# Kernel optimization log

Hardware: AMD Instinct MI355X
Metric: run time of the kernel (lower is better)

## Reference

```python
import jax, jax.numpy as jnp
import numpy as np

# Structure matrix S (n_hos*n_types=6, n_structures=8) and internal int_S (unused in forward)
S_MAT = np.array([[1,0,1,0,0,1,0,1],[0,1,0,1,1,0,0,0],[1,1,0,0,0,0,1,0],[0,0,1,1,0,1,0,0],[0,1,1,0,1,0,0,1],[1,0,0,0,1,0,1,0]], dtype=np.float32)
CONTROL_STRENGTH = 10.0  # self.control_strength
PDHG_ITERS = 150         # fixed-iteration batched primal-dual LP solver
BATCH = 32768
N_STRUCT = 8
N_COMBO = 6


def setup_inputs() -> dict:
    key = jax.random.key(0)
    ks = jax.random.split(key, 9)
    X = jax.random.uniform(ks[0], (BATCH, 2, 3), jnp.float32)  # nonnegative bids
    def lin(k, fan_in, fan_out):
        return jax.random.normal(k, (fan_in, fan_out), jnp.float32) * (1.0 / np.sqrt(fan_in))
    W1 = lin(ks[1], 6, 20);  b1 = jnp.zeros((20,), jnp.float32)
    W2 = lin(ks[2], 20, 20); b2 = jnp.zeros((20,), jnp.float32)
    W3 = lin(ks[3], 20, 20); b3 = jnp.zeros((20,), jnp.float32)
    W4 = lin(ks[4], 20, 8);  b4 = jnp.zeros((8,), jnp.float32)
    S = jnp.asarray(S_MAT)
    return {"X": X, "W1": W1, "b1": b1, "W2": W2, "b2": b2, "W3": W3, "b3": b3,
            "W4": W4, "b4": b4, "S": S, "batch_size": BATCH}


def _mlp(Z, W1, b1, W2, b2, W3, b3, W4, b4):
    h = jnp.tanh(Z @ W1 + b1)
    h = jnp.tanh(h @ W2 + b2)
    h = jnp.tanh(h @ W3 + b3)
    return h @ W4 + b4  # [B, 8]


def _batched_lp(S, z, bvec):
    """Solve, per batch row: max 1'x - c*||x - z||_2  s.t. x>=0, S x <= b.
    Equivalent polytope A x <= b' with A=[S; -I], b'=[b; 0]; solved with PDHG.
    z, bvec: [B, 8], [B, 6]."""
    B = z.shape[0]
    A = jnp.concatenate([S, -jnp.eye(N_STRUCT, dtype=S.dtype)], axis=0)  # [14, 8]
    bfull = jnp.concatenate([bvec, jnp.zeros((B, N_STRUCT), bvec.dtype)], axis=1)  # [B, 14]
    L = jnp.linalg.norm(A)  # Frobenius norm upper-bounds spectral norm
    tau = 1.0 / L
    sigma = 1.0 / L

    def prox_g(v):
        # prox of g(x) = -1'x + c||x - z||_2 (w = ones): shift by tau*w then shrink toward z
        u = v + tau
        d = u - z
        n = jnp.linalg.norm(d, axis=-1, keepdims=True)
        scale = jnp.maximum(0.0, 1.0 - tau * CONTROL_STRENGTH / jnp.maximum(n, 1e-12))
        return z + scale * d

    x0 = jnp.maximum(z, 0.0)
    y0 = jnp.zeros((B, N_COMBO + N_STRUCT), z.dtype)

    def step(carry, _):
        x, xbar, y = carry
        y = jnp.maximum(0.0, y + sigma * (xbar @ A.T - bfull))  # dual ascent + proj >= 0
        x_new = prox_g(x - tau * (y @ A))                        # primal prox step
        return (x_new, 2.0 * x_new - x, y), None

    (x, _, _), _ = jax.lax.scan(step, (x0, x0, y0), None, length=PDHG_ITERS)
    return x


def reference(X, W1, b1, W2, b2, W3, b3, W4, b4, S, batch_size):
    B = X.shape[0]
    Z = X.reshape(B, N_COMBO)              # view(-1, n_hos*n_types)
    z = _mlp(Z, W1, b1, W2, b2, W3, b3, W4, b4)  # neural_net_forward -> [B, 8]
    x1 = _batched_lp(S, z, Z)              # linear_program_forward (W = ones)
    return x1
```

## Files before the change

kernel.cpp:

```cpp
#include <hip/hip_runtime.h>
#include <math.h>


#define N_ITERS 150
typedef float f2 __attribute__((ext_vector_type(2)));
typedef float f4 __attribute__((ext_vector_type(4)));

__device__ __forceinline__ float fast_tanh(float a) {
    float e = __expf(2.0f * a);
    return 1.0f - 2.0f * __builtin_amdgcn_rcpf(e + 1.0f);
}

__device__ __forceinline__ float dpp_swap(float v) {
    union { float f; int i; } u;
    u.f = v;
    u.i = __builtin_amdgcn_update_dpp(0, u.i, 0xB1, 0xF, 0xF, true);
    return u.f;
}

__global__ void __launch_bounds__(64)
__attribute__((amdgpu_waves_per_eu(2)))
matchnet_kernel(
    const float* __restrict__ X,
    const float* __restrict__ W1, const float* __restrict__ b1,
    const float* __restrict__ W2, const float* __restrict__ b2,
    const float* __restrict__ W3, const float* __restrict__ b3,
    const float* __restrict__ W4, const float* __restrict__ b4,
    float* __restrict__ out, int B)
{
    __shared__ alignas(16) float tW1[160], tW2[400], tW3[400], tW4[160];
    __shared__ alignas(16) float sb1[20], sb2[20], sb3[20], sb4[8];
    {
        int tid = threadIdx.x;
        for (int idx = tid; idx < 120; idx += 64) { int i = idx / 20, j = idx % 20; tW1[j * 8 + i] = W1[idx]; }
        for (int idx = tid; idx < 400; idx += 64) { int i = idx / 20, j = idx % 20; tW2[j * 20 + i] = W2[idx]; }
        for (int idx = tid; idx < 400; idx += 64) { int i = idx / 20, j = idx % 20; tW3[j * 20 + i] = W3[idx]; }
        for (int idx = tid; idx < 160; idx += 64) { int i = idx / 8,  k = idx % 8;  tW4[k * 20 + i] = W4[idx]; }
        if (tid < 20) { sb1[tid] = b1[tid]; sb2[tid] = b2[tid]; sb3[tid] = b3[tid]; }
        if (tid < 8) sb4[tid] = b4[tid];
    }
    __syncthreads();

    int gidx = blockIdx.x * blockDim.x + threadIdx.x;
    int row  = gidx >> 2;
    if (row >= B) return;
    int sub = gidx & 3;
    const bool isOdd = (sub & 1) != 0;
    const bool isPairA = (sub < 2);
    const int jb = isOdd ? 10 : 0;
    const int kb = isOdd ? 4 : 0;

    float bb0 = X[row * 6 + 0], bb1 = X[row * 6 + 1], bb2 = X[row * 6 + 2];
    float bb3 = X[row * 6 + 3], bb4 = X[row * 6 + 4], bb5 = X[row * 6 + 5];

    float hA[10], hB[10];
    {
        float acc[10];
        const f2* bv = (const f2*)&sb1[jb];
        #pragma unroll
        for (int p = 0; p < 5; p++) { f2 b = bv[p]; acc[2 * p] = b.x; acc[2 * p + 1] = b.y; }
        #pragma unroll
        for (int n = 0; n < 10; n++) {
            int j = jb + n;
            f4 w0 = *(const f4*)&tW1[j * 8];
            f2 w1 = *(const f2*)&tW1[j * 8 + 4];
            float a = acc[n];
            a = fmaf(bb0, w0.x, a); a = fmaf(bb1, w0.y, a); a = fmaf(bb2, w0.z, a);
            a = fmaf(bb3, w0.w, a); a = fmaf(bb4, w1.x, a); a = fmaf(bb5, w1.y, a);
            acc[n] = fast_tanh(a);
        }
        #pragma unroll
        for (int n = 0; n < 10; n++) {
            float t = dpp_swap(acc[n]);
            hA[n] = isOdd ? t : acc[n];
            hB[n] = isOdd ? acc[n] : t;
        }
    }
    #pragma unroll
    for (int layer = 0; layer < 2; layer++) {
        const float* tw = layer ? tW3 : tW2;
        const float* sb = layer ? sb3 : sb2;
        float acc[10];
        const f2* bv = (const f2*)&sb[jb];
        #pragma unroll
        for (int p = 0; p < 5; p++) { f2 b = bv[p]; acc[2 * p] = b.x; acc[2 * p + 1] = b.y; }
        #pragma unroll
        for (int n = 0; n < 10; n++) {
            int j = jb + n;
            const f4* w = (const f4*)&tw[j * 20];
            f4 w0 = w[0], w1 = w[1], w2 = w[2], w3 = w[3], w4 = w[4];
            float a = acc[n];
            a = fmaf(hA[0], w0.x, a); a = fmaf(hA[1], w0.y, a);
            a = fmaf(hA[2], w0.z, a); a = fmaf(hA[3], w0.w, a);
            a = fmaf(hA[4], w1.x, a); a = fmaf(hA[5], w1.y, a);
            a = fmaf(hA[6], w1.z, a); a = fmaf(hA[7], w1.w, a);
            a = fmaf(hA[8], w2.x, a); a = fmaf(hA[9], w2.y, a);
            a = fmaf(hB[0], w2.z, a); a = fmaf(hB[1], w2.w, a);
            a = fmaf(hB[2], w3.x, a); a = fmaf(hB[3], w3.y, a);
            a = fmaf(hB[4], w3.z, a); a = fmaf(hB[5], w3.w, a);
            a = fmaf(hB[6], w4.x, a); a = fmaf(hB[7], w4.y, a);
            a = fmaf(hB[8], w4.z, a); a = fmaf(hB[9], w4.w, a);
            acc[n] = fast_tanh(a);
        }
        #pragma unroll
        for (int n = 0; n < 10; n++) {
            float t = dpp_swap(acc[n]);
            hA[n] = isOdd ? t : acc[n];
            hB[n] = isOdd ? acc[n] : t;
        }
    }
    float oz0, oz1, oz2, oz3;
    {
        f4 b = *(const f4*)&sb4[kb];
        float acc[4] = {b.x, b.y, b.z, b.w};
        #pragma unroll
        for (int n = 0; n < 4; n++) {
            int k = kb + n;
            const f4* w = (const f4*)&tW4[k * 20];
            f4 w0 = w[0], w1 = w[1], w2 = w[2], w3 = w[3], w4 = w[4];
            float a = acc[n];
            a = fmaf(hA[0], w0.x, a); a = fmaf(hA[1], w0.y, a);
            a = fmaf(hA[2], w0.z, a); a = fmaf(hA[3], w0.w, a);
            a = fmaf(hA[4], w1.x, a); a = fmaf(hA[5], w1.y, a);
            a = fmaf(hA[6], w1.z, a); a = fmaf(hA[7], w1.w, a);
            a = fmaf(hA[8], w2.x, a); a = fmaf(hA[9], w2.y, a);
            a = fmaf(hB[0], w2.z, a); a = fmaf(hB[1], w2.w, a);
            a = fmaf(hB[2], w3.x, a); a = fmaf(hB[3], w3.y, a);
            a = fmaf(hB[4], w3.z, a); a = fmaf(hB[5], w3.w, a);
            a = fmaf(hB[6], w4.x, a); a = fmaf(hB[7], w4.y, a);
            a = fmaf(hB[8], w4.z, a); a = fmaf(hB[9], w4.w, a);
            acc[n] = a;
        }
        oz0 = acc[0]; oz1 = acc[1]; oz2 = acc[2]; oz3 = acc[3];
    }

    const float tau  = 0.18898223650461363f;
    const float c    = 0.03571428571428571f;
    const float tauC = 1.8898223650461363f;

    float ot0 = tau - oz0, ot1 = tau - oz1, ot2 = tau - oz2, ot3 = tau - oz3;
    float oTI0 = ot0, oTI1 = ot1, oTI2 = ot2, oTI3 = ot3;

    float ox0 = fmaxf(oz0, 0.f), ox1 = fmaxf(oz1, 0.f);
    float ox2 = fmaxf(oz2, 0.f), ox3 = fmaxf(oz3, 0.f);
    float oxb0 = ox0, oxb1 = ox1, oxb2 = ox2, oxb3 = ox3;

    float cb0 = c * bb0, cb1 = c * bb1, cb2 = c * bb2;
    float cb3 = c * bb3, cb4 = c * bb4, cb5 = c * bb5;
    float cbq0 = isOdd ? cb4 : cb0;
    float cbq1 = isOdd ? cb3 : cb2;
    float cbq2 = isOdd ? cb5 : cb1;
    float Yq0 = 0.f, Yq1 = 0.f, Yq2 = 0.f;

    #pragma unroll 1
    for (int it = 0; it < N_ITERS; it++) {
        float rxb0 = dpp_swap(oxb0), rxb1 = dpp_swap(oxb1);
        float rxb2 = dpp_swap(oxb2), rxb3 = dpp_swap(oxb3);

        float op_a = oxb0 + rxb1;
        float op_b = oxb2 + rxb3;
        float op_c = oxb3 + rxb2;
        float op_d = isOdd ? op_c : op_b;
        float sq0  = op_a + op_d;
        float op_e = oxb1 + rxb2;
        float op_f = isOdd ? rxb3 : oxb0;
        float sq1  = op_e + op_f;
        float op_g = oxb1 + oxb3;
        float op_h = oxb0 + oxb2;
        float op_i = isOdd ? op_h : op_g;
        float sq2  = op_i + rxb0;

        Yq0 = fmaxf(0.f, fmaf(c, sq0, Yq0) - cbq0);
        Yq1 = fmaxf(0.f, fmaf(c, sq1, Yq1) - cbq1);
        Yq2 = fmaxf(0.f, fmaf(c, sq2, Yq2) - cbq2);

        float rY0 = dpp_swap(Yq0), rY1 = dpp_swap(Yq1), rY2 = dpp_swap(Yq2);

        float op_j = Yq0 + rY2;
        float op_k = isOdd ? Yq2 : Yq1;
        float colq0 = op_j + op_k;
        float op_l = Yq1 + rY0;
        float op_p = isOdd ? 0.f : Yq2;
        float colq1 = op_l + op_p;
        float op_m = Yq0 + rY0;
        float op_n = rY1 + Yq2;
        float op_o = op_m + rY1;
        float colq2 = isOdd ? op_n : op_o;
        float colq3 = isOdd ? op_m : op_n;

        oTI0 = fmaxf(ot0, fmaf(-c, oxb0, oTI0));
        oTI1 = fmaxf(ot1, fmaf(-c, oxb1, oTI1));
        oTI2 = fmaxf(ot2, fmaf(-c, oxb2, oTI2));
        oTI3 = fmaxf(ot3, fmaf(-c, oxb3, oTI3));

        float od0 = (ox0 + oTI0) - colq0;
        float od1 = (ox1 + oTI1) - colq1;
        float od2 = (ox2 + oTI2) - colq2;
        float od3 = (ox3 + oTI3) - colq3;

        float nl = od0 * od0;
        nl = fmaf(od1, od1, nl);
        nl = fmaf(od2, od2, nl);
        nl = fmaf(od3, od3, nl);
        float rn = dpp_swap(nl);
        float nsq = nl + rn;

        float rs = __builtin_amdgcn_rsqf(nsq);
        float scale = fmaxf(0.f, fmaf(-tauC, rs, 1.f));

        float xn0 = fmaf(scale, od0, oz0);
        float xn1 = fmaf(scale, od1, oz1);
        float xn2 = fmaf(scale, od2, oz2);
        float xn3 = fmaf(scale, od3, oz3);
        oxb0 = fmaf(2.f, xn0, -ox0); ox0 = xn0;
        oxb1 = fmaf(2.f, xn1, -ox1); ox1 = xn1;
        oxb2 = fmaf(2.f, xn2, -ox2); ox2 = xn2;
        oxb3 = fmaf(2.f, xn3, -ox3); ox3 = xn3;
    }

    if (isPairA) {
        float4* out4 = (float4*)out;
        out4[row * 2 + (isOdd ? 1 : 0)] = make_float4(ox0, ox1, ox2, ox3);
    }
}

extern "C" void kernel_launch(void* const* d_in, const int* in_sizes, int n_in,
                              void* d_out, int out_size, void* d_ws, size_t ws_size,
                              hipStream_t stream) {
    const float* X  = (const float*)d_in[0];
    const float* W1 = (const float*)d_in[1];
    const float* b1 = (const float*)d_in[2];
    const float* W2 = (const float*)d_in[3];
    const float* b2 = (const float*)d_in[4];
    const float* W3 = (const float*)d_in[5];
    const float* b3 = (const float*)d_in[6];
    const float* W4 = (const float*)d_in[7];
    const float* b4 = (const float*)d_in[8];
    float* out = (float*)d_out;

    int B = in_sizes[0] / 6;
    const int block = 64;
    long long threads = (long long)B * 4;
    int grid = (int)((threads + block - 1) / block);
    hipLaunchKernelGGL(matchnet_kernel, dim3(grid), dim3(block), 0, stream,
                       X, W1, b1, W2, b2, W3, b3, W4, b4, out, B);
}
```

Before: 118.6 us.

## Split PDHG iteration across four lanes per row with quad DPP permutes

Before, the four lanes of a row did redundant work in pairs: each pair held 4 primal components, and two lanes repeated the same computation. The PDHG loop now spreads each row's 8 primal and 6 dual variables across all four lanes, two primal and up to two dual per lane, using quad-permute DPP moves for the A and A^T products and for the norm reduction. This cuts per-lane ALU work in the serial 150-iteration loop. In exchange it adds more cross-lane permutes and per-lane selects, and the waves-per-EU hint now also sets a maximum of 2.

After: 111.9 us. -5.7%, faster.

```diff
diff --git a/kernel.cpp b/kernel.cpp
--- a/kernel.cpp
+++ b/kernel.cpp
@@ -11,15 +11,17 @@
     return 1.0f - 2.0f * __builtin_amdgcn_rcpf(e + 1.0f);
 }
 
-__device__ __forceinline__ float dpp_swap(float v) {
+template <int CTRL>
+__device__ __forceinline__ float qperm(float v) {
     union { float f; int i; } u;
     u.f = v;
-    u.i = __builtin_amdgcn_update_dpp(0, u.i, 0xB1, 0xF, 0xF, true);
+    u.i = __builtin_amdgcn_update_dpp(0, u.i, CTRL, 0xF, 0xF, true);
     return u.f;
 }
+#define QP(a,b,c,d) ((a) | ((b)<<2) | ((c)<<4) | ((d)<<6))
 
 __global__ void __launch_bounds__(64)
-__attribute__((amdgpu_waves_per_eu(2)))
+__attribute__((amdgpu_waves_per_eu(2, 2)))
 matchnet_kernel(
     const float* __restrict__ X,
     const float* __restrict__ W1, const float* __restrict__ b1,
@@ -44,11 +46,17 @@
     int gidx = blockIdx.x * blockDim.x + threadIdx.x;
     int row  = gidx >> 2;
     if (row >= B) return;
-    int sub = gidx & 3;
-    const bool isOdd = (sub & 1) != 0;
-    const bool isPairA = (sub < 2);
-    const int jb = isOdd ? 10 : 0;
-    const int kb = isOdd ? 4 : 0;
+    const int  sub     = gidx & 3;
+    const bool pairOdd = (sub & 1) != 0;
+    const bool isL1  = (sub == 1);
+    const bool isL2  = (sub == 2);
+    const bool isL3  = (sub == 3);
+    const bool isL12 = (sub == 1) || (sub == 2);
+    const bool isL23 = (sub >= 2);
+    const bool isL13 = isL1 || isL3;
+    const bool notL0 = (sub != 0);
+    const int jb = pairOdd ? 10 : 0;
+    const int kb = pairOdd ? 4 : 0;
 
     float bb0 = X[row * 6 + 0], bb1 = X[row * 6 + 1], bb2 = X[row * 6 + 2];
     float bb3 = X[row * 6 + 3], bb4 = X[row * 6 + 4], bb5 = X[row * 6 + 5];
@@ -71,9 +79,9 @@
         }
         #pragma unroll
         for (int n = 0; n < 10; n++) {
-            float t = dpp_swap(acc[n]);
-            hA[n] = isOdd ? t : acc[n];
-            hB[n] = isOdd ? acc[n] : t;
+            float t = qperm<QP(1,0,3,2)>(acc[n]);
+            hA[n] = pairOdd ? t : acc[n];
+            hB[n] = pairOdd ? acc[n] : t;
         }
     }
     #pragma unroll
@@ -104,9 +112,9 @@
         }
         #pragma unroll
         for (int n = 0; n < 10; n++) {
-            float t = dpp_swap(acc[n]);
-            hA[n] = isOdd ? t : acc[n];
-            hB[n] = isOdd ? acc[n] : t;
+            float t = qperm<QP(1,0,3,2)>(acc[n]);
+            hA[n] = pairOdd ? t : acc[n];
+            hB[n] = pairOdd ? acc[n] : t;
         }
     }
     float oz0, oz1, oz2, oz3;
@@ -134,94 +142,88 @@
         oz0 = acc[0]; oz1 = acc[1]; oz2 = acc[2]; oz3 = acc[3];
     }
 
+    float za, zb;
+    {
+        float dZ1 = qperm<QP(0,0,3,3)>(oz2);
+        float dZ2 = qperm<QP(3,3,3,3)>(oz0);
+        float t   = isL3 ? oz2 : oz0;
+        t  = isL1 ? dZ1 : t;
+        za = isL2 ? dZ2 : t;
+        float dZ3 = qperm<QP(0,0,0,0)>(oz3);
+        float dZ4 = qperm<QP(3,3,3,3)>(oz1);
+        float u   = isL3 ? oz3 : oz1;
+        u  = isL1 ? dZ3 : u;
+        zb = isL2 ? dZ4 : u;
+    }
+
     const float tau  = 0.18898223650461363f;
     const float c    = 0.03571428571428571f;
     const float tauC = 1.8898223650461363f;
 
-    float ot0 = tau - oz0, ot1 = tau - oz1, ot2 = tau - oz2, ot3 = tau - oz3;
-    float oTI0 = ot0, oTI1 = ot1, oTI2 = ot2, oTI3 = ot3;
-
-    float ox0 = fmaxf(oz0, 0.f), ox1 = fmaxf(oz1, 0.f);
-    float ox2 = fmaxf(oz2, 0.f), ox3 = fmaxf(oz3, 0.f);
-    float oxb0 = ox0, oxb1 = ox1, oxb2 = ox2, oxb3 = ox3;
-
     float cb0 = c * bb0, cb1 = c * bb1, cb2 = c * bb2;
     float cb3 = c * bb3, cb4 = c * bb4, cb5 = c * bb5;
-    float cbq0 = isOdd ? cb4 : cb0;
-    float cbq1 = isOdd ? cb3 : cb2;
-    float cbq2 = isOdd ? cb5 : cb1;
-    float Yq0 = 0.f, Yq1 = 0.f, Yq2 = 0.f;
+    float cb1q = isL1 ? cb1 : cb0;  cb1q = isL2 ? cb4 : cb1q;  cb1q = isL3 ? cb5 : cb1q;
+    float cb2q = isL1 ? cb3 : cb2;
+
+    float ta = tau - za, tb = tau - zb;
+    float TIa = ta, TIb = tb;
+    float xa = fmaxf(za, 0.f), xb_ = fmaxf(zb, 0.f);
+    float xba = xa, xbb = xb_;
+    float Y1 = 0.f, Y2 = 0.f;
 
     #pragma unroll 1
     for (int it = 0; it < N_ITERS; it++) {
-        float rxb0 = dpp_swap(oxb0), rxb1 = dpp_swap(oxb1);
-        float rxb2 = dpp_swap(oxb2), rxb3 = dpp_swap(oxb3);
-
-        float op_a = oxb0 + rxb1;
-        float op_b = oxb2 + rxb3;
-        float op_c = oxb3 + rxb2;
-        float op_d = isOdd ? op_c : op_b;
-        float sq0  = op_a + op_d;
-        float op_e = oxb1 + rxb2;
-        float op_f = isOdd ? rxb3 : oxb0;
-        float sq1  = op_e + op_f;
-        float op_g = oxb1 + oxb3;
-        float op_h = oxb0 + oxb2;
-        float op_i = isOdd ? op_h : op_g;
-        float sq2  = op_i + rxb0;
-
-        Yq0 = fmaxf(0.f, fmaf(c, sq0, Yq0) - cbq0);
-        Yq1 = fmaxf(0.f, fmaf(c, sq1, Yq1) - cbq1);
-        Yq2 = fmaxf(0.f, fmaf(c, sq2, Yq2) - cbq2);
-
-        float rY0 = dpp_swap(Yq0), rY1 = dpp_swap(Yq1), rY2 = dpp_swap(Yq2);
-
-        float op_j = Yq0 + rY2;
-        float op_k = isOdd ? Yq2 : Yq1;
-        float colq0 = op_j + op_k;
-        float op_l = Yq1 + rY0;
-        float op_p = isOdd ? 0.f : Yq2;
-        float colq1 = op_l + op_p;
-        float op_m = Yq0 + rY0;
-        float op_n = rY1 + Yq2;
-        float op_o = op_m + rY1;
-        float colq2 = isOdd ? op_n : op_o;
-        float colq3 = isOdd ? op_m : op_n;
-
-        oTI0 = fmaxf(ot0, fmaf(-c, oxb0, oTI0));
-        oTI1 = fmaxf(ot1, fmaf(-c, oxb1, oTI1));
-        oTI2 = fmaxf(ot2, fmaf(-c, oxb2, oTI2));
-        oTI3 = fmaxf(ot3, fmaf(-c, oxb3, oTI3));
-
-        float od0 = (ox0 + oTI0) - colq0;
-        float od1 = (ox1 + oTI1) - colq1;
-        float od2 = (ox2 + oTI2) - colq2;
-        float od3 = (ox3 + oTI3) - colq3;
-
-        float nl = od0 * od0;
-        nl = fmaf(od1, od1, nl);
-        nl = fmaf(od2, od2, nl);
-        nl = fmaf(od3, od3, nl);
-        float rn = dpp_swap(nl);
-        float nsq = nl + rn;
+        float dA1 = qperm<QP(1,2,1,0)>(xba);
+        float dA2 = qperm<QP(2,2,2,2)>(xba);
+        float dB1 = qperm<QP(2,0,0,0)>(xbb);
+        float dB2 = qperm<QP(3,3,3,3)>(xbb);
+        float P = isL1 ? xbb : xba;
+        float R = isL3 ? dA2 : dB1;
+        float T = isL13 ? 0.f : dB2;
+        float s1 = (P + dA1) + (R + T);
+        float dA3 = qperm<QP(3,3,3,3)>(xba);
+        float dB3 = qperm<QP(2,2,2,2)>(xbb);
+        float V = isL1 ? dB3 : dA3;
+        float s2 = (xba + xbb) + V;
+
+        Y1 = fmaxf(0.f, fmaf(c, s1, Y1) - cb1q);
+        Y2 = fmaxf(0.f, fmaf(c, s2, Y2) - cb2q);
+
+        float gYa = qperm<QP(3,0,1,0)>(Y1);
+        float gYb = qperm<QP(1,2,3,2)>(Y1);
+        float gYc = qperm<QP(2,2,0,0)>(Y1);
+        float gY2 = qperm<QP(1,0,1,0)>(Y2);
+        float T1 = isL12 ? gYa : Y1;  T1 = isL3 ? gY2 : T1;
+        float T2 = isL23 ? Y1  : Y2;
+        float T3 = isL12 ? gYb : gYa; T3 = isL3 ? 0.f : T3;
+        float colA = (T1 + T2) + T3;
+        float U1 = isL1 ? Y1  : gYb;  U1 = isL2 ? gYc : U1;  U1 = isL3 ? gYa : U1;
+        float U2 = isL2 ? gY2 : Y2;   U2 = isL3 ? gYb : U2;
+        float U3 = notL0 ? 0.f : gYc;
+        float colB = (U1 + U2) + U3;
+
+        TIa = fmaxf(ta, fmaf(-c, xba, TIa));
+        TIb = fmaxf(tb, fmaf(-c, xbb, TIb));
+
+        float da = (xa  + TIa) - colA;
+        float db = (xb_ + TIb) - colB;
+
+        float p  = fmaf(db, db, da * da);
+        float pp = p + qperm<QP(1,0,3,2)>(p);
+        float nsq = pp + qperm<QP(2,3,0,1)>(pp);
 
         float rs = __builtin_amdgcn_rsqf(nsq);
         float scale = fmaxf(0.f, fmaf(-tauC, rs, 1.f));
 
-        float xn0 = fmaf(scale, od0, oz0);
-        float xn1 = fmaf(scale, od1, oz1);
-        float xn2 = fmaf(scale, od2, oz2);
-        float xn3 = fmaf(scale, od3, oz3);
-        oxb0 = fmaf(2.f, xn0, -ox0); ox0 = xn0;
-        oxb1 = fmaf(2.f, xn1, -ox1); ox1 = xn1;
-        oxb2 = fmaf(2.f, xn2, -ox2); ox2 = xn2;
-        oxb3 = fmaf(2.f, xn3, -ox3); ox3 = xn3;
-    }
-
-    if (isPairA) {
-        float4* out4 = (float4*)out;
-        out4[row * 2 + (isOdd ? 1 : 0)] = make_float4(ox0, ox1, ox2, ox3);
-    }
+        float xna = fmaf(scale, da, za);
+        float xnb = fmaf(scale, db, zb);
+        xba = fmaf(2.f, xna, -xa);  xa  = xna;
+        xbb = fmaf(2.f, xnb, -xb_); xb_ = xnb;
+    }
+
+    f2* out2 = (f2*)out;
+    f2 vo; vo.x = xa; vo.y = xb_;
+    out2[gidx] = vo;
 }
 
 extern "C" void kernel_launch(void* const* d_in, const int* in_sizes, int n_in,
```
